# Kernel optimization log

Measured on AMD Instinct MI355X. Metric: run time of the kernel, lower is better.

## Reference

```python
import jax, jax.numpy as jnp
import numpy as np

D_MODEL = 512
BINS = 64


def setup_inputs() -> dict:
    key = jax.random.key(0)
    ks = jax.random.split(key, 5)
    x = jax.random.normal(ks[0], (1, 512, D_MODEL), dtype=jnp.float32)
    # torch Linear(2d, d): weight [d, 2d]; store transposed [2d, d] for x @ W
    s1 = 1.0 / np.sqrt(2 * D_MODEL)
    W1 = jax.random.uniform(ks[1], (2 * D_MODEL, D_MODEL), jnp.float32, -s1, s1)
    b1 = jax.random.uniform(ks[2], (D_MODEL,), jnp.float32, -s1, s1)
    s2 = 1.0 / np.sqrt(D_MODEL)
    W2 = jax.random.uniform(ks[3], (D_MODEL, BINS), jnp.float32, -s2, s2)
    b2 = jax.random.uniform(ks[4], (BINS,), jnp.float32, -s2, s2)
    return {"x": x, "W1": W1, "b1": b1, "W2": W2, "b2": b2}


def reference(x, W1, b1, W2, b2):
    # pair = cat([xi, xj], -1); Linear(cat) == xi @ W1[:d] + xj @ W1[d:]
    # This factorization is exact and avoids materializing the [B,N,N,2d] tensor.
    d = x.shape[-1]
    hi = jnp.einsum('bnd,de->bne', x, W1[:d])      # [B, N, d]
    hj = jnp.einsum('bnd,de->bne', x, W1[d:])      # [B, N, d]
    h = hi[:, :, None, :] + hj[:, None, :, :] + b1  # [B, N, N, d]
    h = jax.nn.gelu(h, approximate=False)           # torch nn.GELU default is exact
    return jnp.einsum('bijd,de->bije', h, W2) + b2  # [B, N, N, bins]
```

## Files before the change

kernel.cpp:

```cpp
#include <hip/hip_runtime.h>
#include <hip/hip_fp16.h>

#define D 512
#define NTOK 512
#define BINS 64

typedef float v4f __attribute__((ext_vector_type(4)));
typedef int v4i __attribute__((ext_vector_type(4)));
typedef short short8 __attribute__((ext_vector_type(8)));
typedef _Float16 h8 __attribute__((ext_vector_type(8)));

__device__ __forceinline__ __half2 gelu2(__half2 x) {
    __half2 s = __hmul2(x, x);
    __half2 q = __hmul2(x, __hfma2(s, __float2half2_rn(-0.1029437f),
                                      __float2half2_rn(-2.3022082f)));
    __half2 e = h2exp2(q);
    __half2 r = h2rcp(__hadd2(e, __float2half2_rn(1.0f)));
    return __hmul2(x, r);
}

__device__ __forceinline__ __half2 bc_h2(int v) { return __builtin_bit_cast(__half2, v); }
__device__ __forceinline__ int bc_i(__half2 v) { return __builtin_bit_cast(int, v); }

__device__ __forceinline__ v4i pack8(v4f a, v4f b) {
    h8 o;
    o[0] = (_Float16)a.x; o[1] = (_Float16)a.y; o[2] = (_Float16)a.z; o[3] = (_Float16)a.w;
    o[4] = (_Float16)b.x; o[5] = (_Float16)b.y; o[6] = (_Float16)b.z; o[7] = (_Float16)b.w;
    return __builtin_bit_cast(v4i, o);
}

__device__ __forceinline__ void g2lds16(const void* g, void* l) {
    __builtin_amdgcn_global_load_lds(
        (const __attribute__((address_space(1))) void*)g,
        (__attribute__((address_space(3))) void*)l, 16, 0, 0);
}

#define WAITVM_(N) asm volatile("s_waitcnt vmcnt(" #N ")" ::: "memory")
#define WAITVM(N) WAITVM_(N)

__global__ __launch_bounds__(256) void k_pack(const float* __restrict__ x,
                                              const float* __restrict__ W1,
                                              const float* __restrict__ W2,
                                              v4i* __restrict__ Ap,
                                              v4i* __restrict__ Wp,
                                              short8* __restrict__ Bp) {
    const int b = blockIdx.x;
    const int t = threadIdx.x;
    if (b < 32) {
        const int rb = b;
#pragma unroll
        for (int u = 0; u < 4; ++u) {
            const int e = t + 256 * u;
            const int l = e & 63, ks = e >> 6;
            const float* src = x + (size_t)(rb * 16 + (l & 15)) * D + ks * 32 + (l >> 4) * 8;
            v4f a = *(const v4f*)src;
            v4f c = *(const v4f*)(src + 4);
            Ap[(size_t)(rb * 16 + ks) * 64 + l] = pack8(a, c);
        }
    } else if (b < 288) {
        const int slot = (b - 32) * 256 + t;
        const int l = slot & 63;
        const int ks = (slot >> 6) & 15;
        const int nb = slot >> 10;
        const int ng = nb * 16 + (l & 15);
        const float* src = W1 + (size_t)((ng >> 9) * D + ks * 32 + (l >> 4) * 8) * D
                              + (ng & 511);
        h8 o;
#pragma unroll
        for (int j = 0; j < 8; ++j) o[j] = (_Float16)src[(size_t)j * D];
        Wp[(size_t)(nb * 16 + ks) * 64 + l] = __builtin_bit_cast(v4i, o);
    } else {
        const int tid = (b - 288) * 256 + t;
        const int ll = tid & 63;
        const int nt = (tid >> 6) & 3;
        const int kt = tid >> 8;
        const int colp = nt * 16 + (ll & 15);
        const int krow = kt * 32 + (ll >> 4) * 8;
        short8 v;
#pragma unroll
        for (int u = 0; u < 8; ++u) {
            _Float16 hv = (_Float16)W2[(size_t)(krow + u) * BINS + colp];
            v[u] = __builtin_bit_cast(short, hv);
        }
        Bp[tid] = v;
    }
}

__global__ __launch_bounds__(256) void k_gemm(const v4i* __restrict__ Ap,
                                              const v4i* __restrict__ Wp,
                                              const float* __restrict__ b1,
                                              _Float16* __restrict__ hi,
                                              _Float16* __restrict__ hj) {
    const int l = threadIdx.x & 63;
    const int w = threadIdx.x >> 6;
    const int c = l & 15;
    const int q = l >> 4;
    const int mb = blockIdx.x >> 4;
    const int cb = blockIdx.x & 15;
    const int nb = cb * 4 + w;

    const v4i* ap = Ap + (size_t)mb * 16 * 64 + l;
    const v4i* wp = Wp + (size_t)nb * 16 * 64 + l;

    v4f acc = {0.f, 0.f, 0.f, 0.f};
#pragma unroll
    for (int ks = 0; ks < 16; ++ks) {
        v4i a0 = ap[ks * 64];
        v4i bb = wp[ks * 64];
        acc = __builtin_amdgcn_mfma_f32_16x16x32_f16(__builtin_bit_cast(h8, a0),
                                                     __builtin_bit_cast(h8, bb), acc, 0, 0, 0);
    }

    const int ng = nb * 16 + c;
    const float b1v = (ng < D) ? b1[ng] : 0.0f;
    _Float16* dst = (ng < D ? hi : hj) + (ng & 511);
    const int row0 = mb * 16 + q * 4;
#pragma unroll
    for (int r = 0; r < 4; ++r)
        dst[(size_t)(row0 + r) * D] = (_Float16)(acc[r] + b1v);
}

#define NBUF 6
#define BUFSZ 6144
__global__ __launch_bounds__(256, 4) void k_main(const __half* __restrict__ hi,
                                                 const __half* __restrict__ hj,
                                                 const float* __restrict__ b2,
                                                 const char* __restrict__ BpB,
                                                 float* __restrict__ out) {
    const int l = threadIdx.x & 63;
    const int w = threadIdx.x >> 6;
    const int c = l & 15;
    const int q = l >> 4;
    const int ib = (blockIdx.x >> 5) * 16;
    const int j0 = (blockIdx.x & 31) * 16;

    __shared__ __align__(16) char lds[NBUF * BUFSZ];

    const char* hjB = (const char*)hj;
    const char* hiB = (const char*)hi;

#define STAGE(kt_, bi_)                                                          \
    {                                                                            \
        char* buf_ = lds + (bi_) * BUFSZ;                                        \
        g2lds16(BpB + (size_t)(kt_) * 4096 + (w * 64 + l) * 16, buf_ + w * 1024);\
        if (w == 0)                                                              \
            g2lds16(hjB + (size_t)(j0 + (l & 15)) * 1024 + (kt_) * 64 + (l >> 4) * 16, \
                    buf_ + 4096);                                                \
        if (w == 1)                                                              \
            g2lds16(hiB + (size_t)(ib + (l >> 2)) * 1024 + (kt_) * 64 + (l & 3) * 16,  \
                    buf_ + 5120);                                                \
    }

    v4f acc[4][4] = {};

    STAGE(0, 0) STAGE(1, 1)

#pragma unroll
    for (int ph = 0; ph < 8; ++ph) {
        const int kt0 = ph * 2;
        if (ph < 7) { STAGE(kt0 + 2, (kt0 + 2) % NBUF) STAGE(kt0 + 3, (kt0 + 3) % NBUF) }
        if (ph < 7) {
            if (w < 2) WAITVM(4); else WAITVM(2);
        } else {
            WAITVM(0);
        }
        __builtin_amdgcn_s_barrier();

#pragma unroll
        for (int kk = 0; kk < 2; ++kk) {
            const int kt = kt0 + kk;
            const char* buf = lds + (kt % NBUF) * BUFSZ;
            const v4i* bsec = (const v4i*)buf;
            v4i bfr[4];
#pragma unroll
            for (int nt = 0; nt < 4; ++nt) bfr[nt] = bsec[nt * 64 + l];
            v4i hjraw = ((const v4i*)(buf + 4096))[l];
            __half2 j0h = bc_h2(hjraw.x), j1h = bc_h2(hjraw.y);
            __half2 j2h = bc_h2(hjraw.z), j3h = bc_h2(hjraw.w);
#pragma unroll
            for (int p = 0; p < 4; ++p) {
                v4i ar = *(const v4i*)(buf + 5120 + ((w * 4 + p) * 4 + q) * 16);
                __half2 g0 = gelu2(__hadd2(bc_h2(ar.x), j0h));
                __half2 g1 = gelu2(__hadd2(bc_h2(ar.y), j1h));
                __half2 g2 = gelu2(__hadd2(bc_h2(ar.z), j2h));
                __half2 g3 = gelu2(__hadd2(bc_h2(ar.w), j3h));
                v4i ai = {bc_i(g0), bc_i(g1), bc_i(g2), bc_i(g3)};
                h8 af = __builtin_bit_cast(h8, ai);
#pragma unroll
                for (int nt = 0; nt < 4; ++nt)
                    acc[p][nt] = __builtin_amdgcn_mfma_f32_16x16x32_f16(
                        af, __builtin_bit_cast(h8, bfr[nt]), acc[p][nt], 0, 0, 0);
            }
        }
    }
#undef STAGE

    const int i0 = ib + w * 4;
#pragma unroll
    for (int p = 0; p < 4; ++p) {
        const size_t rowbase = ((size_t)(i0 + p) * NTOK + j0 + q * 4) * BINS;
#pragma unroll
        for (int nt = 0; nt < 4; ++nt) {
            const float bb = b2[nt * 16 + c];
            float* op = out + rowbase + nt * 16 + c;
#pragma unroll
            for (int rr = 0; rr < 4; ++rr)
                op[(size_t)rr * BINS] = acc[p][nt][rr] + bb;
        }
    }
}

extern "C" void kernel_launch(void* const* d_in, const int* in_sizes, int n_in,
                              void* d_out, int out_size, void* d_ws, size_t ws_size,
                              hipStream_t stream) {
    const float* x  = (const float*)d_in[0];
    const float* W1 = (const float*)d_in[1];
    const float* b1 = (const float*)d_in[2];
    const float* W2 = (const float*)d_in[3];
    const float* b2 = (const float*)d_in[4];
    float* out = (float*)d_out;

    char* ws = (char*)d_ws;
    __half* hi = (__half*)ws;
    __half* hj = (__half*)(ws + (512u << 10));
    short8* Bp = (short8*)(ws + (1u << 20));
    v4i*    Ap = (v4i*)(ws + (1u << 20) + (64u << 10));
    v4i*    Wp = (v4i*)(ws + (1u << 20) + (64u << 10) + (512u << 10));

    k_pack<<<304, 256, 0, stream>>>(x, W1, W2, Ap, Wp, Bp);
    k_gemm<<<512, 256, 0, stream>>>(Ap, Wp, b1, (_Float16*)hi, (_Float16*)hj);
    k_main<<<1024, 256, 0, stream>>>(hi, hj, b2, (const char*)Bp, out);
}
```

Measured before the change: 122.8 us.

## Fuse input packing into projection GEMM with LDS-staged triple-buffered loads

Removes the separate pack pass for x and W1 and the intermediate Ap/Wp buffers. The projection kernel now streams fp32 x and W1 tiles straight into LDS via global_load_lds with a 3-stage pipeline and a swizzled layout, converting to fp16 on read. This drops one kernel launch and a round trip through global memory. In exchange it adds more LDS traffic, per-element conversion work and a more complex synchronization scheme.

Measured after the change: 122.4 us. Within noise of the previous version (-0.3%).

```diff
diff --git a/kernel.cpp b/kernel.cpp
--- a/kernel.cpp
+++ b/kernel.cpp
@@ -22,13 +22,6 @@
 __device__ __forceinline__ __half2 bc_h2(int v) { return __builtin_bit_cast(__half2, v); }
 __device__ __forceinline__ int bc_i(__half2 v) { return __builtin_bit_cast(int, v); }
 
-__device__ __forceinline__ v4i pack8(v4f a, v4f b) {
-    h8 o;
-    o[0] = (_Float16)a.x; o[1] = (_Float16)a.y; o[2] = (_Float16)a.z; o[3] = (_Float16)a.w;
-    o[4] = (_Float16)b.x; o[5] = (_Float16)b.y; o[6] = (_Float16)b.z; o[7] = (_Float16)b.w;
-    return __builtin_bit_cast(v4i, o);
-}
-
 __device__ __forceinline__ void g2lds16(const void* g, void* l) {
     __builtin_amdgcn_global_load_lds(
         (const __attribute__((address_space(1))) void*)g,
@@ -38,39 +31,17 @@
 #define WAITVM_(N) asm volatile("s_waitcnt vmcnt(" #N ")" ::: "memory")
 #define WAITVM(N) WAITVM_(N)
 
-__global__ __launch_bounds__(256) void k_pack(const float* __restrict__ x,
-                                              const float* __restrict__ W1,
-                                              const float* __restrict__ W2,
-                                              v4i* __restrict__ Ap,
-                                              v4i* __restrict__ Wp,
-                                              short8* __restrict__ Bp) {
+__global__ __launch_bounds__(256, 2) void k_proj(const float* __restrict__ x,
+                                                 const float* __restrict__ W1,
+                                                 const float* __restrict__ b1,
+                                                 const float* __restrict__ W2,
+                                                 _Float16* __restrict__ hi,
+                                                 _Float16* __restrict__ hj,
+                                                 short8* __restrict__ Bp) {
     const int b = blockIdx.x;
     const int t = threadIdx.x;
-    if (b < 32) {
-        const int rb = b;
-#pragma unroll
-        for (int u = 0; u < 4; ++u) {
-            const int e = t + 256 * u;
-            const int l = e & 63, ks = e >> 6;
-            const float* src = x + (size_t)(rb * 16 + (l & 15)) * D + ks * 32 + (l >> 4) * 8;
-            v4f a = *(const v4f*)src;
-            v4f c = *(const v4f*)(src + 4);
-            Ap[(size_t)(rb * 16 + ks) * 64 + l] = pack8(a, c);
-        }
-    } else if (b < 288) {
-        const int slot = (b - 32) * 256 + t;
-        const int l = slot & 63;
-        const int ks = (slot >> 6) & 15;
-        const int nb = slot >> 10;
-        const int ng = nb * 16 + (l & 15);
-        const float* src = W1 + (size_t)((ng >> 9) * D + ks * 32 + (l >> 4) * 8) * D
-                              + (ng & 511);
-        h8 o;
-#pragma unroll
-        for (int j = 0; j < 8; ++j) o[j] = (_Float16)src[(size_t)j * D];
-        Wp[(size_t)(nb * 16 + ks) * 64 + l] = __builtin_bit_cast(v4i, o);
-    } else {
-        const int tid = (b - 288) * 256 + t;
+    if (b >= 512) {
+        const int tid = (b - 512) * 256 + t;
         const int ll = tid & 63;
         const int nt = (tid >> 6) & 3;
         const int kt = tid >> 8;
@@ -83,41 +54,74 @@
             v[u] = __builtin_bit_cast(short, hv);
         }
         Bp[tid] = v;
-    }
-}
-
-__global__ __launch_bounds__(256) void k_gemm(const v4i* __restrict__ Ap,
-                                              const v4i* __restrict__ Wp,
-                                              const float* __restrict__ b1,
-                                              _Float16* __restrict__ hi,
-                                              _Float16* __restrict__ hj) {
-    const int l = threadIdx.x & 63;
-    const int w = threadIdx.x >> 6;
+        return;
+    }
+    const int l = t & 63;
+    const int w = t >> 6;
     const int c = l & 15;
     const int q = l >> 4;
-    const int mb = blockIdx.x >> 4;
-    const int cb = blockIdx.x & 15;
-    const int nb = cb * 4 + w;
-
-    const v4i* ap = Ap + (size_t)mb * 16 * 64 + l;
-    const v4i* wp = Wp + (size_t)nb * 16 * 64 + l;
+    const int gm = b >> 4;
+    const int gn = b & 15;
+    const int m0 = gm * 16;
+    const int halfBase = (gn >> 3) * 512;
+    const int ncol0 = (gn & 7) * 64;
+    const int nn = w * 16 + c;
+
+    __shared__ __align__(16) char lds[3 * 20480];
+
+#define PSTAGE(c_, bi_)                                                           \
+    {                                                                             \
+        char* buf_ = lds + (bi_) * 20480;                                         \
+        g2lds16(x + (size_t)(m0 + (l & 15)) * 512 + (c_) * 64                     \
+                    + (w >> 1) * 32 + (l >> 4) * 8 + (w & 1) * 4,                 \
+                buf_ + w * 1024);                                                 \
+        _Pragma("unroll")                                                         \
+        for (int jj = 0; jj < 4; ++jj) {                                          \
+            const int j_ = w * 4 + jj;                                            \
+            g2lds16(W1 + (size_t)(halfBase + (c_) * 64 + j_ * 4 + (l >> 4)) * 512 \
+                        + ncol0 + (((l & 15) ^ ((j_ >> 1) & 7)) << 2),            \
+                    buf_ + 4096 + j_ * 1024);                                     \
+        }                                                                         \
+    }
+
+    const int cb0 = ((((nn >> 2) ^ (q & 7)) << 4) | ((nn & 3) << 2));
+    const int cb1 = ((((nn >> 2) ^ ((4 + q) & 7)) << 4) | ((nn & 3) << 2));
 
     v4f acc = {0.f, 0.f, 0.f, 0.f};
-#pragma unroll
-    for (int ks = 0; ks < 16; ++ks) {
-        v4i a0 = ap[ks * 64];
-        v4i bb = wp[ks * 64];
-        acc = __builtin_amdgcn_mfma_f32_16x16x32_f16(__builtin_bit_cast(h8, a0),
-                                                     __builtin_bit_cast(h8, bb), acc, 0, 0, 0);
-    }
-
-    const int ng = nb * 16 + c;
-    const float b1v = (ng < D) ? b1[ng] : 0.0f;
-    _Float16* dst = (ng < D ? hi : hj) + (ng & 511);
-    const int row0 = mb * 16 + q * 4;
+
+    PSTAGE(0, 0)
+#pragma unroll
+    for (int ch = 0; ch < 8; ++ch) {
+        if (ch < 7) PSTAGE(ch + 1, (ch + 1) % 3)
+        if (ch < 7) WAITVM(5); else WAITVM(0);
+        __builtin_amdgcn_s_barrier();
+
+        const char* buf = lds + (ch % 3) * 20480;
+#pragma unroll
+        for (int ks = 0; ks < 2; ++ks) {
+            v4f a0 = *(const v4f*)(buf + ks * 2048 + l * 16);
+            v4f a1 = *(const v4f*)(buf + ks * 2048 + 1024 + l * 16);
+            h8 af;
+            af[0] = (_Float16)a0.x; af[1] = (_Float16)a0.y;
+            af[2] = (_Float16)a0.z; af[3] = (_Float16)a0.w;
+            af[4] = (_Float16)a1.x; af[5] = (_Float16)a1.y;
+            af[6] = (_Float16)a1.z; af[7] = (_Float16)a1.w;
+            const char* wb = buf + 4096 + (ks * 32 + q * 8) * 256
+                           + (ks ? cb1 : cb0);
+            h8 bf;
+#pragma unroll
+            for (int j = 0; j < 8; ++j)
+                bf[j] = (_Float16)(*(const float*)(wb + j * 256));
+            acc = __builtin_amdgcn_mfma_f32_16x16x32_f16(af, bf, acc, 0, 0, 0);
+        }
+    }
+#undef PSTAGE
+
+    const float b1v = (gn < 8) ? b1[ncol0 + nn] : 0.0f;
+    _Float16* dst = (gn < 8 ? hi : hj) + ncol0 + nn;
 #pragma unroll
     for (int r = 0; r < 4; ++r)
-        dst[(size_t)(row0 + r) * D] = (_Float16)(acc[r] + b1v);
+        dst[(size_t)(m0 + q * 4 + r) * 512] = (_Float16)(acc[r] + b1v);
 }
 
 #define NBUF 6
@@ -221,13 +225,11 @@
     float* out = (float*)d_out;
 
     char* ws = (char*)d_ws;
-    __half* hi = (__half*)ws;
-    __half* hj = (__half*)(ws + (512u << 10));
-    short8* Bp = (short8*)(ws + (1u << 20));
-    v4i*    Ap = (v4i*)(ws + (1u << 20) + (64u << 10));
-    v4i*    Wp = (v4i*)(ws + (1u << 20) + (64u << 10) + (512u << 10));
-
-    k_pack<<<304, 256, 0, stream>>>(x, W1, W2, Ap, Wp, Bp);
-    k_gemm<<<512, 256, 0, stream>>>(Ap, Wp, b1, (_Float16*)hi, (_Float16*)hj);
-    k_main<<<1024, 256, 0, stream>>>(hi, hj, b2, (const char*)Bp, out);
-}
+    _Float16* hi = (_Float16*)ws;
+    _Float16* hj = (_Float16*)(ws + (512u << 10));
+    short8*   Bp = (short8*)(ws + (1u << 20));
+
+    k_proj<<<528, 256, 0, stream>>>(x, W1, b1, W2, hi, hj, Bp);
+    k_main<<<1024, 256, 0, stream>>>((const __half*)hi, (const __half*)hj, b2,
+                                     (const char*)Bp, out);
+}
```
